# Optimization experiments

Hardware: AMD Instinct MI355X
Metric: run time of the kernel (lower is better)

The kernel has to match this reference:

```python
import jax, jax.numpy as jnp
import numpy as np

D_MODEL = 1024
N_HEADS = 16
D_K = D_MODEL // N_HEADS


def setup_inputs() -> dict:
    key = jax.random.key(0)
    ks = jax.random.split(key, 11)
    B, S = 2, 2048
    scale = 1.0 / np.sqrt(D_MODEL)
    return {
        "query": jax.random.normal(ks[0], (B, S, D_MODEL), jnp.float32),
        "key": jax.random.normal(ks[1], (B, S, D_MODEL), jnp.float32),
        "value": jax.random.normal(ks[2], (B, S, D_MODEL), jnp.float32),
        "w_q": jax.random.normal(ks[3], (D_MODEL, D_MODEL), jnp.float32) * scale,
        "b_q": jnp.zeros((D_MODEL,), jnp.float32),
        "w_k": jax.random.normal(ks[4], (D_MODEL, D_MODEL), jnp.float32) * scale,
        "b_k": jnp.zeros((D_MODEL,), jnp.float32),
        "w_v": jax.random.normal(ks[5], (D_MODEL, D_MODEL), jnp.float32) * scale,
        "b_v": jnp.zeros((D_MODEL,), jnp.float32),
        "w_o": jax.random.normal(ks[6], (D_MODEL, D_MODEL), jnp.float32) * scale,
        "b_o": jnp.zeros((D_MODEL,), jnp.float32),
    }


def reference(query, key, value, w_q, b_q, w_k, b_k, w_v, b_v, w_o, b_o):
    B, S, _ = query.shape
    # Linear projections (torch Linear: x @ W.T + b), split heads -> (B, H, S, Dk)
    def proj(x, w, b):
        y = jnp.einsum('bsd,ed->bse', x, w) + b
        return y.reshape(B, -1, N_HEADS, D_K).transpose(0, 2, 1, 3)
    q = proj(query, w_q, b_q)
    k = proj(key, w_k, b_k)
    v = proj(value, w_v, b_v)
    # Scaled dot-product attention (full O(S^2) scores, faithful to source)
    scores = jnp.einsum('bhqd,bhkd->bhqk', q, k) / np.sqrt(D_K)
    attn = jax.nn.softmax(scores, axis=-1)
    out = jnp.einsum('bhqk,bhkd->bhqd', attn, v)  # (B, H, S, Dk)
    out = out.transpose(0, 2, 1, 3).reshape(B, S, D_MODEL)
    out = jnp.einsum('bsd,ed->bse', out, w_o) + b_o
    return out
```

## Files before the change

### kernel.cpp

```cpp
#include <hip/hip_runtime.h>
#include <hip/hip_bf16.h>

#define DM 1024
#define NH 16
#define DKH 64
#define BB 2
#define SS 2048
#define MM (BB*SS)

typedef __bf16 v8bf __attribute__((ext_vector_type(8)));
typedef float  v4f  __attribute__((ext_vector_type(4)));
typedef float  v16f __attribute__((ext_vector_type(16)));

__device__ __forceinline__ unsigned short f2bf(float f) {
    union { float f; unsigned int u; } v; v.f = f;
    unsigned int u = v.u;
    unsigned int r = (u + 0x7fffu + ((u >> 16) & 1u)) >> 16;
    return (unsigned short)r;
}

__device__ __forceinline__ int cvtpk(float lo, float hi) {
    int r;
    asm("v_cvt_pk_bf16_f32 %0, %1, %2" : "=v"(r) : "v"(lo), "v"(hi));
    return r;
}

__device__ __forceinline__ void pl32swap(int& a, int& b) {
    asm("v_permlane32_swap_b32 %0, %1" : "+v"(a), "+v"(b));
}

__device__ __forceinline__ void gl16(const unsigned short* g, unsigned short* l) {
    auto gp = reinterpret_cast<const __attribute__((address_space(1))) unsigned int*>(
        reinterpret_cast<uintptr_t>(g));
    auto lp = reinterpret_cast<__attribute__((address_space(3))) unsigned int*>(
        reinterpret_cast<uintptr_t>(l));
    __builtin_amdgcn_global_load_lds(gp, lp, 16, 0, 0);
}

__global__ __launch_bounds__(256) void cvt_to_bf16(
    const float* __restrict__ xq, const float* __restrict__ xk, const float* __restrict__ xv,
    const float* __restrict__ wq, const float* __restrict__ wk, const float* __restrict__ wv,
    const float* __restrict__ wo, unsigned short* __restrict__ dst)
{
    const int y = blockIdx.y;
    const float* src;
    size_t n, off;
    if (y < 3) {
        src = (y == 0) ? xq : (y == 1) ? xk : xv;
        n = (size_t)MM * DM;
        off = (size_t)y * MM * DM;
    } else {
        src = (y == 3) ? wq : (y == 4) ? wk : (y == 5) ? wv : wo;
        n = (size_t)DM * DM;
        off = (size_t)3 * MM * DM + (size_t)(y - 3) * DM * DM;
    }
    unsigned short* d = dst + off;
    const size_t stride = (size_t)gridDim.x * blockDim.x;
    for (size_t i = (size_t)blockIdx.x * blockDim.x + threadIdx.x; i * 8 < n; i += stride) {
        float4 a = ((const float4*)src)[2 * i];
        float4 b = ((const float4*)src)[2 * i + 1];
        uint4 o;
        o.x = (unsigned)cvtpk(a.x, a.y);
        o.y = (unsigned)cvtpk(a.z, a.w);
        o.z = (unsigned)cvtpk(b.x, b.y);
        o.w = (unsigned)cvtpk(b.z, b.w);
        ((uint4*)d)[i] = o;
    }
}

__global__ __launch_bounds__(256) void proj_qkv_b(
    const unsigned short* __restrict__ xb, const unsigned short* __restrict__ wb,
    const float* __restrict__ bq, const float* __restrict__ bk, const float* __restrict__ bv,
    unsigned short* __restrict__ q_ws, unsigned short* __restrict__ k_ws,
    unsigned short* __restrict__ vt_ws)
{
    const int z = blockIdx.z;
    const unsigned short* X = xb + (size_t)z * MM * DM;
    const unsigned short* W = wb + (size_t)z * DM * DM;
    const float* bias = (z == 0) ? bq : (z == 1) ? bk : bv;

    __shared__ unsigned short lA[128 * 32];
    __shared__ unsigned short lB[128 * 32];

    const int t = threadIdx.x;
    const int lane = t & 63, w = t >> 6;
    const int wm = w >> 1, wn = w & 1;
    const int g = lane >> 4, lr = lane & 15;

    const int orig = blockIdx.y * 8 + blockIdx.x;
    const int swz = (orig & 7) * 32 + (orig >> 3);
    const int mbase = (swz >> 3) * 128;
    const int nbase = (swz & 7) * 128;

    const int srow = lane >> 2;
    const int scol = (lane & 3) * 8;

    v4f acc[4][4];
#pragma unroll
    for (int i = 0; i < 4; ++i)
#pragma unroll
        for (int j = 0; j < 4; ++j)
            acc[i][j] = (v4f){0.f, 0.f, 0.f, 0.f};

    for (int kb = 0; kb < DM; kb += 32) {
        __syncthreads();
        gl16(X + (size_t)(mbase + w * 16 + srow) * DM + kb + scol,       &lA[w * 512]);
        gl16(X + (size_t)(mbase + 64 + w * 16 + srow) * DM + kb + scol,  &lA[(w + 4) * 512]);
        gl16(W + (size_t)(nbase + w * 16 + srow) * DM + kb + scol,       &lB[w * 512]);
        gl16(W + (size_t)(nbase + 64 + w * 16 + srow) * DM + kb + scol,  &lB[(w + 4) * 512]);
        __syncthreads();

        v8bf af[4], bf[4];
#pragma unroll
        for (int mt = 0; mt < 4; ++mt)
            af[mt] = *(const v8bf*)(&lA[(wm * 64 + mt * 16 + lr) * 32 + g * 8]);
#pragma unroll
        for (int nt = 0; nt < 4; ++nt)
            bf[nt] = *(const v8bf*)(&lB[(wn * 64 + nt * 16 + lr) * 32 + g * 8]);
#pragma unroll
        for (int mt = 0; mt < 4; ++mt)
#pragma unroll
            for (int nt = 0; nt < 4; ++nt)
                acc[mt][nt] = __builtin_amdgcn_mfma_f32_16x16x32_bf16(af[mt], bf[nt], acc[mt][nt], 0, 0, 0);
    }

    const float scale = (z == 0) ? 0.18033688011112042f : 1.0f;
#pragma unroll
    for (int nt = 0; nt < 4; ++nt) {
        int e = nbase + wn * 64 + nt * 16 + lr;
        float bval = bias[e];
        int h = e >> 6, dk = e & 63;
#pragma unroll
        for (int mt = 0; mt < 4; ++mt) {
#pragma unroll
            for (int r = 0; r < 4; ++r) {
                int m = mbase + wm * 64 + mt * 16 + g * 4 + r;
                float val = (acc[mt][nt][r] + bval) * scale;
                unsigned short o = f2bf(val);
                int b = m >> 11, s = m & 2047;
                if (z == 2) {
                    vt_ws[((size_t)(b * NH + h) * DKH + dk) * SS + s] = o;
                } else {
                    unsigned short* dst = (z == 0) ? q_ws : k_ws;
                    dst[((size_t)(b * NH + h) * SS + s) * DKH + dk] = o;
                }
            }
        }
    }
}

#define KB 64
#define LDP 72
#define BUFS 4608

__global__ __launch_bounds__(256) void attn_kernel(
    const unsigned short* __restrict__ q_ws, const unsigned short* __restrict__ k_ws,
    const unsigned short* __restrict__ vt_ws, unsigned short* __restrict__ o_ws)
{
    __shared__ unsigned short lsBuf[2 * 2 * BUFS];

    const int t = threadIdx.x, l = t & 63, w = t >> 6;
    const int h = l >> 5, ql = l & 31;
    const int id = blockIdx.x;
    const int swzb = (id & 7) * 64 + (id >> 3);
    const int bh = swzb >> 4, qb = swzb & 15;
    const int q0 = qb * 128 + w * 32;

    const unsigned short* Kbase = k_ws + (size_t)bh * SS * DKH;
    const unsigned short* Vbase = vt_ws + (size_t)bh * DKH * SS;

    v8bf qf[4];
#pragma unroll
    for (int c = 0; c < 4; ++c)
        qf[c] = *(const v8bf*)(q_ws + ((size_t)bh * SS + q0 + ql) * DKH + c * 16 + h * 8);

    v16f oT[2];
#pragma unroll
    for (int d = 0; d < 2; ++d)
#pragma unroll
        for (int r = 0; r < 16; ++r) oT[d][r] = 0.f;
    float l_lane = 0.f;
    const v16f z16 = {};

    const int r0 = t >> 3, c0 = (t & 7) * 8;
    uint4 kst0, kst1, vst0, vst1;

    kst0 = *(const uint4*)(Kbase + (size_t)(r0)      * DKH + c0);
    kst1 = *(const uint4*)(Kbase + (size_t)(r0 + 32) * DKH + c0);
    vst0 = *(const uint4*)(Vbase + (size_t)(r0)      * SS + c0);
    vst1 = *(const uint4*)(Vbase + (size_t)(r0 + 32) * SS + c0);
    {
        unsigned short* Kp = lsBuf;
        unsigned short* Vp = lsBuf + BUFS;
        *(uint4*)&Kp[r0 * LDP + c0] = kst0;
        *(uint4*)&Kp[(r0 + 32) * LDP + c0] = kst1;
        *(uint4*)&Vp[r0 * LDP + c0] = vst0;
        *(uint4*)&Vp[(r0 + 32) * LDP + c0] = vst1;
    }
    kst0 = *(const uint4*)(Kbase + (size_t)(KB + r0)      * DKH + c0);
    kst1 = *(const uint4*)(Kbase + (size_t)(KB + r0 + 32) * DKH + c0);
    vst0 = *(const uint4*)(Vbase + (size_t)(r0)      * SS + KB + c0);
    vst1 = *(const uint4*)(Vbase + (size_t)(r0 + 32) * SS + KB + c0);
    __syncthreads();

    const int NT = SS / KB;
    int p = 0;
    for (int tt = 0; tt < NT; ++tt) {
        unsigned short* Kp = lsBuf + p * (2 * BUFS);
        unsigned short* Vp = Kp + BUFS;
        if (tt + 1 < NT) {
            unsigned short* Kn = lsBuf + (p ^ 1) * (2 * BUFS);
            unsigned short* Vn = Kn + BUFS;
            *(uint4*)&Kn[r0 * LDP + c0] = kst0;
            *(uint4*)&Kn[(r0 + 32) * LDP + c0] = kst1;
            *(uint4*)&Vn[r0 * LDP + c0] = vst0;
            *(uint4*)&Vn[(r0 + 32) * LDP + c0] = vst1;
        }
        if (tt + 2 < NT) {
            int kt2 = (tt + 2) * KB;
            kst0 = *(const uint4*)(Kbase + (size_t)(kt2 + r0)      * DKH + c0);
            kst1 = *(const uint4*)(Kbase + (size_t)(kt2 + r0 + 32) * DKH + c0);
            vst0 = *(const uint4*)(Vbase + (size_t)(r0)      * SS + kt2 + c0);
            vst1 = *(const uint4*)(Vbase + (size_t)(r0 + 32) * SS + kt2 + c0);
        }

        v16f sT[2];
        __builtin_amdgcn_s_setprio(1);
#pragma unroll
        for (int kb = 0; kb < 2; ++kb) {
            v8bf kf = *(const v8bf*)&Kp[(kb * 32 + ql) * LDP + h * 8];
            sT[kb] = __builtin_amdgcn_mfma_f32_32x32x16_bf16(kf, qf[0], z16, 0, 0, 0);
        }
#pragma unroll
        for (int c = 1; c < 4; ++c)
#pragma unroll
            for (int kb = 0; kb < 2; ++kb) {
                v8bf kf = *(const v8bf*)&Kp[(kb * 32 + ql) * LDP + c * 16 + h * 8];
                sT[kb] = __builtin_amdgcn_mfma_f32_32x32x16_bf16(kf, qf[c], sT[kb], 0, 0, 0);
            }
        __builtin_amdgcn_s_setprio(0);

        float rs0 = 0.f, rs1 = 0.f, rs2 = 0.f, rs3 = 0.f;
#pragma unroll
        for (int kb = 0; kb < 2; ++kb)
#pragma unroll
            for (int r = 0; r < 16; r += 4) {
                float e0 = __builtin_amdgcn_exp2f(sT[kb][r + 0]);
                float e1 = __builtin_amdgcn_exp2f(sT[kb][r + 1]);
                float e2 = __builtin_amdgcn_exp2f(sT[kb][r + 2]);
                float e3 = __builtin_amdgcn_exp2f(sT[kb][r + 3]);
                sT[kb][r + 0] = e0; sT[kb][r + 1] = e1;
                sT[kb][r + 2] = e2; sT[kb][r + 3] = e3;
                rs0 += e0; rs1 += e1; rs2 += e2; rs3 += e3;
            }
        l_lane += (rs0 + rs1) + (rs2 + rs3);

        v8bf pfrag[4];
#pragma unroll
        for (int c = 0; c < 4; ++c) {
            const int cc = c & 1, kb = c >> 1;
            int A0 = cvtpk(sT[kb][8 * cc + 0], sT[kb][8 * cc + 1]);
            int A1 = cvtpk(sT[kb][8 * cc + 2], sT[kb][8 * cc + 3]);
            int B0 = cvtpk(sT[kb][8 * cc + 4], sT[kb][8 * cc + 5]);
            int B1 = cvtpk(sT[kb][8 * cc + 6], sT[kb][8 * cc + 7]);
            pl32swap(A0, B0);
            pl32swap(A1, B1);
            union { int i[4]; v8bf v; } u;
            u.i[0] = A0; u.i[1] = A1; u.i[2] = B0; u.i[3] = B1;
            pfrag[c] = u.v;
        }

        __builtin_amdgcn_s_setprio(1);
#pragma unroll
        for (int db = 0; db < 2; ++db)
#pragma unroll
            for (int c = 0; c < 4; ++c) {
                v8bf vf = *(const v8bf*)&Vp[(db * 32 + ql) * LDP + c * 16 + h * 8];
                oT[db] = __builtin_amdgcn_mfma_f32_32x32x16_bf16(vf, pfrag[c], oT[db], 0, 0, 0);
            }
        __builtin_amdgcn_s_setprio(0);

        __syncthreads();
        p ^= 1;
    }

    float l_run = l_lane + __shfl_xor(l_lane, 32);
    float inv = 1.0f / l_run;
    unsigned short* lO = lsBuf;
    const int row = w * 32 + ql;
#pragma unroll
    for (int db = 0; db < 2; ++db)
#pragma unroll
        for (int a = 0; a < 4; ++a) {
            int dbase = db * 32 + 8 * a + 4 * h;
            int pk0 = cvtpk(oT[db][4 * a + 0] * inv, oT[db][4 * a + 1] * inv);
            int pk1 = cvtpk(oT[db][4 * a + 2] * inv, oT[db][4 * a + 3] * inv);
            *(unsigned int*)&lO[row * LDP + dbase]     = pk0;
            *(unsigned int*)&lO[row * LDP + dbase + 2] = pk1;
        }
    __syncthreads();

    const int b = bh >> 4, hh = bh & 15;
#pragma unroll
    for (int i = 0; i < 4; ++i) {
        int idx = i * 256 + t;
        int orow = idx >> 3;
        int c8 = (idx & 7) * 8;
        int s = qb * 128 + orow;
        *(uint4*)(o_ws + ((size_t)b * SS + s) * DM + hh * DKH + c8) =
            *(const uint4*)&lO[orow * LDP + c8];
    }
}

__global__ __launch_bounds__(256) void proj_o_b(
    const unsigned short* __restrict__ A, const unsigned short* __restrict__ W,
    const float* __restrict__ bo, float* __restrict__ out)
{
    __shared__ unsigned short lA[128 * 32];
    __shared__ unsigned short lB[128 * 32];

    const int t = threadIdx.x;
    const int lane = t & 63, w = t >> 6;
    const int wm = w >> 1, wn = w & 1;
    const int g = lane >> 4, lr = lane & 15;

    const int orig = blockIdx.y * 8 + blockIdx.x;
    const int swz = (orig & 7) * 32 + (orig >> 3);
    const int mbase = (swz >> 3) * 128;
    const int nbase = (swz & 7) * 128;

    const int srow = lane >> 2;
    const int scol = (lane & 3) * 8;

    v4f acc[4][4];
#pragma unroll
    for (int i = 0; i < 4; ++i)
#pragma unroll
        for (int j = 0; j < 4; ++j)
            acc[i][j] = (v4f){0.f, 0.f, 0.f, 0.f};

    for (int kb = 0; kb < DM; kb += 32) {
        __syncthreads();
        gl16(A + (size_t)(mbase + w * 16 + srow) * DM + kb + scol,       &lA[w * 512]);
        gl16(A + (size_t)(mbase + 64 + w * 16 + srow) * DM + kb + scol,  &lA[(w + 4) * 512]);
        gl16(W + (size_t)(nbase + w * 16 + srow) * DM + kb + scol,       &lB[w * 512]);
        gl16(W + (size_t)(nbase + 64 + w * 16 + srow) * DM + kb + scol,  &lB[(w + 4) * 512]);
        __syncthreads();

        v8bf af[4], bf[4];
#pragma unroll
        for (int mt = 0; mt < 4; ++mt)
            af[mt] = *(const v8bf*)(&lA[(wm * 64 + mt * 16 + lr) * 32 + g * 8]);
#pragma unroll
        for (int nt = 0; nt < 4; ++nt)
            bf[nt] = *(const v8bf*)(&lB[(wn * 64 + nt * 16 + lr) * 32 + g * 8]);
#pragma unroll
        for (int mt = 0; mt < 4; ++mt)
#pragma unroll
            for (int nt = 0; nt < 4; ++nt)
                acc[mt][nt] = __builtin_amdgcn_mfma_f32_16x16x32_bf16(af[mt], bf[nt], acc[mt][nt], 0, 0, 0);
    }

#pragma unroll
    for (int nt = 0; nt < 4; ++nt) {
        int e = nbase + wn * 64 + nt * 16 + lr;
        float bval = bo[e];
#pragma unroll
        for (int mt = 0; mt < 4; ++mt) {
#pragma unroll
            for (int r = 0; r < 4; ++r) {
                int m = mbase + wm * 64 + mt * 16 + g * 4 + r;
                out[(size_t)m * DM + e] = acc[mt][nt][r] + bval;
            }
        }
    }
}

extern "C" void kernel_launch(void* const* d_in, const int* in_sizes, int n_in,
                              void* d_out, int out_size, void* d_ws, size_t ws_size,
                              hipStream_t stream) {
    const float* q  = (const float*)d_in[0];
    const float* k  = (const float*)d_in[1];
    const float* v  = (const float*)d_in[2];
    const float* wq = (const float*)d_in[3];
    const float* bq = (const float*)d_in[4];
    const float* wk = (const float*)d_in[5];
    const float* bk = (const float*)d_in[6];
    const float* wv = (const float*)d_in[7];
    const float* bv = (const float*)d_in[8];
    const float* wo = (const float*)d_in[9];
    const float* bo = (const float*)d_in[10];
    float* out = (float*)d_out;

    unsigned short* ws    = (unsigned short*)d_ws;
    unsigned short* q_ws  = ws;
    unsigned short* k_ws  = q_ws + (size_t)MM * DM;
    unsigned short* vt_ws = k_ws + (size_t)MM * DM;
    unsigned short* xb    = vt_ws + (size_t)MM * DM;
    unsigned short* wb    = xb + (size_t)3 * MM * DM;
    unsigned short* o_ws  = xb;

    cvt_to_bf16<<<dim3(256, 7), 256, 0, stream>>>(q, k, v, wq, wk, wv, wo, xb);
    proj_qkv_b<<<dim3(8, 32, 3), 256, 0, stream>>>(xb, wb, bq, bk, bv, q_ws, k_ws, vt_ws);
    attn_kernel<<<dim3(512), 256, 0, stream>>>(q_ws, k_ws, vt_ws, o_ws);
    proj_o_b<<<dim3(8, 32), 256, 0, stream>>>(o_ws, wb + (size_t)3 * DM * DM, bo, out);
}
```

Baseline: 132.2 us.

## Split attention KV range across wave pairs with swizzled LDS and merge partials

Each attention block now handles 64 queries, with two wave pairs each covering half of the key range. Per-block K/V tiles are loaded through a direct global-to-LDS helper (gl16) into an XOR-swizzled unpadded layout. This replaces the register-staged double buffer with a single buffer and a barrier per step. Partial outputs and row sums are combined through LDS in the epilogue, and the grid doubles to 1024 blocks to raise occupancy. The cost is that the load-compute overlap of the old double buffer is lost, and the epilogue adds an LDS reduction.

```diff
diff --git a/kernel.cpp b/kernel.cpp
--- a/kernel.cpp
+++ b/kernel.cpp
@@ -7,6 +7,7 @@
 #define BB 2
 #define SS 2048
 #define MM (BB*SS)
+#define HKB 1024
 
 typedef __bf16 v8bf __attribute__((ext_vector_type(8)));
 typedef float  v4f  __attribute__((ext_vector_type(4)));
@@ -149,22 +150,21 @@
     }
 }
 
-#define KB 64
-#define LDP 72
-#define BUFS 4608
-
 __global__ __launch_bounds__(256) void attn_kernel(
     const unsigned short* __restrict__ q_ws, const unsigned short* __restrict__ k_ws,
     const unsigned short* __restrict__ vt_ws, unsigned short* __restrict__ o_ws)
 {
-    __shared__ unsigned short lsBuf[2 * 2 * BUFS];
+    __shared__ __align__(16) unsigned short ls[16896];
 
     const int t = threadIdx.x, l = t & 63, w = t >> 6;
     const int h = l >> 5, ql = l & 31;
+    const int qg = w & 1, hf = w >> 1;
+
     const int id = blockIdx.x;
-    const int swzb = (id & 7) * 64 + (id >> 3);
-    const int bh = swzb >> 4, qb = swzb & 15;
-    const int q0 = qb * 128 + w * 32;
+    const int j = id >> 3;
+    const int bh = (id & 7) * 4 + (j & 3);
+    const int qp = j >> 2;
+    const int q0 = qp * 64 + qg * 32;
 
     const unsigned short* Kbase = k_ws + (size_t)bh * SS * DKH;
     const unsigned short* Vbase = vt_ws + (size_t)bh * DKH * SS;
@@ -182,60 +182,39 @@
     float l_lane = 0.f;
     const v16f z16 = {};
 
-    const int r0 = t >> 3, c0 = (t & 7) * 8;
-    uint4 kst0, kst1, vst0, vst1;
-
-    kst0 = *(const uint4*)(Kbase + (size_t)(r0)      * DKH + c0);
-    kst1 = *(const uint4*)(Kbase + (size_t)(r0 + 32) * DKH + c0);
-    vst0 = *(const uint4*)(Vbase + (size_t)(r0)      * SS + c0);
-    vst1 = *(const uint4*)(Vbase + (size_t)(r0 + 32) * SS + c0);
-    {
-        unsigned short* Kp = lsBuf;
-        unsigned short* Vp = lsBuf + BUFS;
-        *(uint4*)&Kp[r0 * LDP + c0] = kst0;
-        *(uint4*)&Kp[(r0 + 32) * LDP + c0] = kst1;
-        *(uint4*)&Vp[r0 * LDP + c0] = vst0;
-        *(uint4*)&Vp[(r0 + 32) * LDP + c0] = vst1;
-    }
-    kst0 = *(const uint4*)(Kbase + (size_t)(KB + r0)      * DKH + c0);
-    kst1 = *(const uint4*)(Kbase + (size_t)(KB + r0 + 32) * DKH + c0);
-    vst0 = *(const uint4*)(Vbase + (size_t)(r0)      * SS + KB + c0);
-    vst1 = *(const uint4*)(Vbase + (size_t)(r0 + 32) * SS + KB + c0);
-    __syncthreads();
-
-    const int NT = SS / KB;
-    int p = 0;
-    for (int tt = 0; tt < NT; ++tt) {
-        unsigned short* Kp = lsBuf + p * (2 * BUFS);
-        unsigned short* Vp = Kp + BUFS;
-        if (tt + 1 < NT) {
-            unsigned short* Kn = lsBuf + (p ^ 1) * (2 * BUFS);
-            unsigned short* Vn = Kn + BUFS;
-            *(uint4*)&Kn[r0 * LDP + c0] = kst0;
-            *(uint4*)&Kn[(r0 + 32) * LDP + c0] = kst1;
-            *(uint4*)&Vn[r0 * LDP + c0] = vst0;
-            *(uint4*)&Vn[(r0 + 32) * LDP + c0] = vst1;
-        }
-        if (tt + 2 < NT) {
-            int kt2 = (tt + 2) * KB;
-            kst0 = *(const uint4*)(Kbase + (size_t)(kt2 + r0)      * DKH + c0);
-            kst1 = *(const uint4*)(Kbase + (size_t)(kt2 + r0 + 32) * DKH + c0);
-            vst0 = *(const uint4*)(Vbase + (size_t)(r0)      * SS + kt2 + c0);
-            vst1 = *(const uint4*)(Vbase + (size_t)(r0 + 32) * SS + kt2 + c0);
-        }
+    const int kv = w & 1, thf = w >> 1;
+    unsigned short* tbase = ls + w * 4096;
+    const int swz0 = (ql ^ (ql >> 3)) & 7;
+    unsigned short* Kp = ls + (hf * 2) * 4096;
+    unsigned short* Vp = ls + (hf * 2 + 1) * 4096;
+
+    for (int st = 0; st < 16; ++st) {
+        const int kt = thf * HKB + st * 64;
+#pragma unroll
+        for (int i = 0; i < 8; ++i) {
+            int row = i * 8 + (l >> 3);
+            int cs = (l & 7) ^ ((row ^ (row >> 3)) & 7);
+            const unsigned short* src = (kv == 0)
+                ? Kbase + (size_t)(kt + row) * DKH + cs * 8
+                : Vbase + (size_t)row * SS + kt + cs * 8;
+            gl16(src, tbase + i * 512);
+        }
+        __syncthreads();
 
         v16f sT[2];
         __builtin_amdgcn_s_setprio(1);
 #pragma unroll
         for (int kb = 0; kb < 2; ++kb) {
-            v8bf kf = *(const v8bf*)&Kp[(kb * 32 + ql) * LDP + h * 8];
+            int sw = swz0 ^ (kb ? 4 : 0);
+            v8bf kf = *(const v8bf*)&Kp[(kb * 32 + ql) * 64 + ((h ^ sw) * 8)];
             sT[kb] = __builtin_amdgcn_mfma_f32_32x32x16_bf16(kf, qf[0], z16, 0, 0, 0);
         }
 #pragma unroll
         for (int c = 1; c < 4; ++c)
 #pragma unroll
             for (int kb = 0; kb < 2; ++kb) {
-                v8bf kf = *(const v8bf*)&Kp[(kb * 32 + ql) * LDP + c * 16 + h * 8];
+                int sw = swz0 ^ (kb ? 4 : 0);
+                v8bf kf = *(const v8bf*)&Kp[(kb * 32 + ql) * 64 + (((c * 2 + h) ^ sw) * 8)];
                 sT[kb] = __builtin_amdgcn_mfma_f32_32x32x16_bf16(kf, qf[c], sT[kb], 0, 0, 0);
             }
         __builtin_amdgcn_s_setprio(0);
@@ -275,41 +254,47 @@
         for (int db = 0; db < 2; ++db)
 #pragma unroll
             for (int c = 0; c < 4; ++c) {
-                v8bf vf = *(const v8bf*)&Vp[(db * 32 + ql) * LDP + c * 16 + h * 8];
+                int sw = swz0 ^ (db ? 4 : 0);
+                v8bf vf = *(const v8bf*)&Vp[(db * 32 + ql) * 64 + (((c * 2 + h) ^ sw) * 8)];
                 oT[db] = __builtin_amdgcn_mfma_f32_32x32x16_bf16(vf, pfrag[c], oT[db], 0, 0, 0);
             }
         __builtin_amdgcn_s_setprio(0);
 
         __syncthreads();
-        p ^= 1;
-    }
-
-    float l_run = l_lane + __shfl_xor(l_lane, 32);
-    float inv = 1.0f / l_run;
-    unsigned short* lO = lsBuf;
-    const int row = w * 32 + ql;
+    }
+
+    float lsum = l_lane + __shfl_xor(l_lane, 32);
+    float* ep = (float*)ls + w * 2080;
 #pragma unroll
     for (int db = 0; db < 2; ++db)
 #pragma unroll
-        for (int a = 0; a < 4; ++a) {
-            int dbase = db * 32 + 8 * a + 4 * h;
-            int pk0 = cvtpk(oT[db][4 * a + 0] * inv, oT[db][4 * a + 1] * inv);
-            int pk1 = cvtpk(oT[db][4 * a + 2] * inv, oT[db][4 * a + 3] * inv);
-            *(unsigned int*)&lO[row * LDP + dbase]     = pk0;
-            *(unsigned int*)&lO[row * LDP + dbase + 2] = pk1;
-        }
+        for (int r = 0; r < 16; ++r) {
+            int d = db * 32 + (r & 3) + 8 * (r >> 2) + 4 * h;
+            ep[ql * 65 + d] = oT[db][r];
+        }
+    if (h == 0) ep[ql * 65 + 64] = lsum;
     __syncthreads();
 
+    const int row = t >> 2;
+    const int ck = t & 3;
+    const int qg2 = row >> 5, qr = row & 31;
+    const float* e0 = (float*)ls + qg2 * 2080 + qr * 65;
+    const float* e1 = (float*)ls + (2 + qg2) * 2080 + qr * 65;
+    const float linv = 1.0f / (e0[64] + e1[64]);
     const int b = bh >> 4, hh = bh & 15;
-#pragma unroll
-    for (int i = 0; i < 4; ++i) {
-        int idx = i * 256 + t;
-        int orow = idx >> 3;
-        int c8 = (idx & 7) * 8;
-        int s = qb * 128 + orow;
-        *(uint4*)(o_ws + ((size_t)b * SS + s) * DM + hh * DKH + c8) =
-            *(const uint4*)&lO[orow * LDP + c8];
-    }
+    unsigned short* op = o_ws + ((size_t)b * SS + qp * 64 + row) * DM + hh * DKH + ck * 16;
+    const int d0 = ck * 16;
+    uint4 o0, o1;
+    o0.x = (unsigned)cvtpk((e0[d0+0]+e1[d0+0])*linv, (e0[d0+1]+e1[d0+1])*linv);
+    o0.y = (unsigned)cvtpk((e0[d0+2]+e1[d0+2])*linv, (e0[d0+3]+e1[d0+3])*linv);
+    o0.z = (unsigned)cvtpk((e0[d0+4]+e1[d0+4])*linv, (e0[d0+5]+e1[d0+5])*linv);
+    o0.w = (unsigned)cvtpk((e0[d0+6]+e1[d0+6])*linv, (e0[d0+7]+e1[d0+7])*linv);
+    o1.x = (unsigned)cvtpk((e0[d0+8]+e1[d0+8])*linv, (e0[d0+9]+e1[d0+9])*linv);
+    o1.y = (unsigned)cvtpk((e0[d0+10]+e1[d0+10])*linv, (e0[d0+11]+e1[d0+11])*linv);
+    o1.z = (unsigned)cvtpk((e0[d0+12]+e1[d0+12])*linv, (e0[d0+13]+e1[d0+13])*linv);
+    o1.w = (unsigned)cvtpk((e0[d0+14]+e1[d0+14])*linv, (e0[d0+15]+e1[d0+15])*linv);
+    *(uint4*)op = o0;
+    *(uint4*)(op + 8) = o1;
 }
 
 __global__ __launch_bounds__(256) void proj_o_b(
@@ -402,6 +387,6 @@
 
     cvt_to_bf16<<<dim3(256, 7), 256, 0, stream>>>(q, k, v, wq, wk, wv, wo, xb);
     proj_qkv_b<<<dim3(8, 32, 3), 256, 0, stream>>>(xb, wb, bq, bk, bv, q_ws, k_ws, vt_ws);
-    attn_kernel<<<dim3(512), 256, 0, stream>>>(q_ws, k_ws, vt_ws, o_ws);
+    attn_kernel<<<dim3(1024), 256, 0, stream>>>(q_ws, k_ws, vt_ws, o_ws);
     proj_o_b<<<dim3(8, 32), 256, 0, stream>>>(o_ws, wb + (size_t)3 * DM * DM, bo, out);
 }
```

After: 141.8 us. 1.07x slower.
